# Kernel optimization log

Measured on AMD Instinct MI355X. Metric: run time of the kernel, lower is better.

Reference implementation:

```python
import jax, jax.numpy as jnp
import numpy as np

N_SPIKES = 1_000_000
N_UNITS = 400
N_NEIGHB = 64
C = 3        # n_candidates
S = 2        # n_search per candidate
E = 1        # n_explore


def setup_inputs() -> dict:
    key = jax.random.key(0)
    k1, k2, k3, k4 = jax.random.split(key, 4)
    top_candidates = jax.random.randint(k1, (N_SPIKES, C), 0, N_UNITS, dtype=jnp.int32)
    unit_search_neighbors = jax.random.randint(k2, (N_UNITS, S), 0, N_UNITS, dtype=jnp.int32)
    neighborhood_ids = jax.random.randint(k3, (N_SPIKES,), 0, N_NEIGHB, dtype=jnp.int32)
    unit_logliks = jax.random.normal(k4, (N_UNITS,), dtype=jnp.float32)
    return {
        "unit_logliks": unit_logliks,
        "top_candidates": top_candidates,
        "unit_search_neighbors": unit_search_neighbors,
        "neighborhood_ids": neighborhood_ids,
    }


def _propose(top, usn, nb):
    """Deterministic JAX version of CandidateSet.propose_candidates.

    top: (n, C) int top candidate units per spike (invariant 1)
    usn: (U, S) int search neighbors per unit
    nb:  (n,)   int neighborhood id per spike
    Returns: candidates (n, C + C*S + E) with dups erased to -1,
             unit_neighborhood_counts (U, N_NEIGHB).
    """
    n = top.shape[0]
    U = usn.shape[0]
    # search candidates: gather neighbors of each top candidate -> (n, C*S)
    search = usn[top].reshape(n, C * S)
    # scatter-add counts of best unit per neighborhood (np.add.at equivalent)
    counts = jnp.zeros((U, N_NEIGHB), jnp.int32).at[top[:, 0], nb].add(1)
    # units_overlapping_neighborhoods: per neighborhood, sorted unit ids with
    # count > 0, padded with sentinel U -> (N_NEIGHB, U)
    overlap = counts.T > 0                                  # (N_NEIGHB, U)
    explore_units = jnp.sort(jnp.where(overlap, jnp.arange(U, dtype=jnp.int32), U), axis=1)
    # searchsorted(row, U) == number of valid entries per neighborhood
    n_explore = overlap.sum(axis=1).astype(jnp.int32)       # (N_NEIGHB,)
    ne = n_explore[nb]                                      # (n,)
    # integers_without_inner_replacement with E=1: uniform index in [0, ne)
    u = jax.random.uniform(jax.random.key(1), (n, E))
    targs = jnp.floor(u * ne[:, None].astype(u.dtype)).astype(jnp.int32)
    targs = jnp.where(ne[:, None] > 0, jnp.minimum(targs, ne[:, None] - 1), -1)
    explore = explore_units[nb[:, None], jnp.maximum(targs, 0)]
    explore = jnp.where(targs < 0, -1, explore)             # (n, E)
    candidates = jnp.concatenate([top, search, explore], axis=1)  # (n, T)
    # second scatter-add: all non-top columns (negatives masked out)
    tail = candidates[:, 1:]
    valid = tail >= 0
    counts = counts.at[jnp.where(valid, tail, 0), jnp.where(valid, nb[:, None], 0)].add(
        valid.astype(jnp.int32)
    )
    # erase_dups: keep first occurrence in each row, later dups -> -1
    T = candidates.shape[1]
    eq = candidates[:, :, None] == candidates[:, None, :]   # (n, T, T)
    earlier = jnp.tril(jnp.ones((T, T), bool), k=-1)        # [j, i] with i < j
    dup = (eq & earlier).any(axis=2)
    candidates = jnp.where(dup, -1, candidates)
    return candidates, counts


def reference(unit_logliks, top_candidates, unit_search_neighbors, neighborhood_ids):
    candidates, counts = _propose(top_candidates, unit_search_neighbors, neighborhood_ids)
    # per-candidate loglik gather (the float gather used by the E step)
    scores = jnp.where(candidates >= 0, unit_logliks[jnp.maximum(candidates, 0)], 0.0)
    return candidates, counts, scores
```

## Files before the change

### kernel.cpp

```cpp
#include <hip/hip_runtime.h>
#include <stdint.h>

#define N_UNITS   400
#define N_NEIGHB  64
#define C         3
#define S         2
#define T         10
#define NSLICE_A  128
#define HALF_NB   32
#define HH        (HALF_NB * N_UNITS)
#define EH        (N_UNITS * 32)
#define BS        256
#define MB        512

__device__ __forceinline__ uint32_t rotl32(uint32_t x, int d) {
    return (x << d) | (x >> (32 - d));
}

__device__ __forceinline__ void threefry_key01(uint32_t x0, uint32_t x1,
                                               uint32_t& o0, uint32_t& o1) {
    const uint32_t ks0 = 0u;
    const uint32_t ks1 = 1u;
    const uint32_t ks2 = 0x1BD11BDBu;
    x0 += ks0; x1 += ks1;
#define TF_RND(r) { x0 += x1; x1 = rotl32(x1, r); x1 ^= x0; }
    TF_RND(13) TF_RND(15) TF_RND(26) TF_RND(6)
    x0 += ks1; x1 += ks2 + 1u;
    TF_RND(17) TF_RND(29) TF_RND(16) TF_RND(24)
    x0 += ks2; x1 += ks0 + 2u;
    TF_RND(13) TF_RND(15) TF_RND(26) TF_RND(6)
    x0 += ks0; x1 += ks1 + 3u;
    TF_RND(17) TF_RND(29) TF_RND(16) TF_RND(24)
    x0 += ks1; x1 += ks2 + 4u;
    TF_RND(13) TF_RND(15) TF_RND(26) TF_RND(6)
    x0 += ks2; x1 += ks0 + 5u;
#undef TF_RND
    o0 = x0; o1 = x1;
}

__device__ __forceinline__ int explore_index(int i, int ne) {
    uint32_t o0, o1;
    threefry_key01(0u, (uint32_t)i, o0, o1);
    uint32_t bits = o0 ^ o1;
    float u = __uint_as_float((bits >> 9) | 0x3F800000u) - 1.0f;
    int t = (int)floorf(u * (float)ne);
    return min(t, ne - 1);
}

__global__ void k_histA(const int* __restrict__ top,
                        const int* __restrict__ nbid,
                        uint32_t* __restrict__ PA, int n, int chunk) {
    __shared__ uint32_t hist[HH];
    for (int k = threadIdx.x; k < HH; k += blockDim.x) hist[k] = 0u;
    __syncthreads();
    int h = blockIdx.x & 1, s = blockIdx.x >> 1;
    int lo = s * chunk, hi = min(n, lo + chunk);
    const int4* top4 = (const int4*)top;
#define PROC(nb, t0, t1, t2) if (((nb) >> 5) == h) { \
    int r = ((nb) & 31) * N_UNITS; \
    atomicAdd(&hist[r + (t0)], 1u); \
    atomicAdd(&hist[r + (t1)], 0x10000u); \
    atomicAdd(&hist[r + (t2)], 0x10000u); }
    for (int i0 = lo + threadIdx.x * 4; i0 < hi; i0 += blockDim.x * 4) {
        if (i0 + 4 <= hi) {
            int4 nb4 = *(const int4*)(nbid + i0);
            int j = (i0 * 3) >> 2;
            int4 ta = top4[j], tb = top4[j + 1], tc = top4[j + 2];
            PROC(nb4.x, ta.x, ta.y, ta.z)
            PROC(nb4.y, ta.w, tb.x, tb.y)
            PROC(nb4.z, tb.z, tb.w, tc.x)
            PROC(nb4.w, tc.y, tc.z, tc.w)
        } else {
            for (int i = i0; i < hi; ++i)
                PROC(nbid[i], top[3 * i], top[3 * i + 1], top[3 * i + 2])
        }
    }
#undef PROC
    __syncthreads();
    uint32_t* Pb = PA + (size_t)blockIdx.x * HH;
    for (int k = threadIdx.x; k < HH; k += blockDim.x) Pb[k] = hist[k];
}

__global__ void k_tables_base(const uint32_t* __restrict__ PA,
                              const int* __restrict__ usn,
                              int* __restrict__ wtbl,
                              int* __restrict__ wne,
                              float* __restrict__ out_counts) {
    __shared__ int scan[512];
    __shared__ int s_c[N_UNITS];
    __shared__ int s_h3[N_UNITS];
    int b = blockIdx.x, u = threadIdx.x;
    int h = b >> 5;
    int base = (b & 31) * N_UNITS;
    int h0 = 0, h12 = 0;
    if (u < N_UNITS) {
#pragma unroll 8
        for (int s = 0; s < NSLICE_A; ++s) {
            uint32_t w = PA[(size_t)(s * 2 + h) * HH + base + u];
            h0  += (int)(w & 0xFFFFu);
            h12 += (int)(w >> 16);
        }
        int h3 = h0 + h12;
        s_h3[u] = h3;
        s_c[u] = h3;
    }
    int p = (u < N_UNITS && h0 > 0) ? 1 : 0;
    scan[u] = p;
    __syncthreads();
    for (int off = 1; off < 512; off <<= 1) {
        int add = (u >= off) ? scan[u - off] : 0;
        __syncthreads();
        scan[u] += add;
        __syncthreads();
    }
    if (p) wtbl[b * N_UNITS + scan[u] - 1] = u;
    if (u == 511) wne[b] = scan[511];
    if (u < N_UNITS) {
        int h3 = s_h3[u];
        if (h3 > 0) {
            int2 nbr = ((const int2*)usn)[u];
            atomicAdd(&s_c[nbr.x], h3);
            atomicAdd(&s_c[nbr.y], h3);
        }
    }
    __syncthreads();
    if (u < N_UNITS)
        out_counts[u * N_NEIGHB + b] = (float)s_c[u];
}

__global__ void k_main(const float* __restrict__ logliks,
                       const int* __restrict__ top,
                       const int* __restrict__ usn,
                       const int* __restrict__ nbid,
                       const int* __restrict__ wtbl,
                       const int* __restrict__ wne,
                       uint32_t* __restrict__ PD,
                       float* __restrict__ out_cand,
                       float* __restrict__ out_scores,
                       int n, int chunk) {
    __shared__ uint32_t hist[EH];
    __shared__ int   s_usn[N_UNITS * S];
    __shared__ float s_ll[N_UNITS];
    __shared__ int   s_ne[N_NEIGHB];
    int tid = threadIdx.x;
    for (int k = tid; k < EH; k += BS) hist[k] = 0u;
    for (int k = tid; k < N_UNITS * S; k += BS) s_usn[k] = usn[k];
    for (int k = tid; k < N_UNITS; k += BS)     s_ll[k]  = logliks[k];
    for (int k = tid; k < N_NEIGHB; k += BS)    s_ne[k]  = wne[k];
    __syncthreads();

    int lo = blockIdx.x * chunk, hi = min(n, lo + chunk);
    for (int i = lo + tid; i < hi; i += BS) {
        int nb = nbid[i];
        int cand[T];
        cand[0] = top[i * 3 + 0];
        cand[1] = top[i * 3 + 1];
        cand[2] = top[i * 3 + 2];
#pragma unroll
        for (int c = 0; c < C; ++c) {
            cand[C + 2 * c]     = s_usn[cand[c] * 2 + 0];
            cand[C + 2 * c + 1] = s_usn[cand[c] * 2 + 1];
        }
        int ne = s_ne[nb];
        if (ne > 0) {
            int t = explore_index(i, ne);
            int ex = wtbl[nb * N_UNITS + t];
            cand[T - 1] = ex;
            atomicAdd(&hist[ex * 32 + (nb >> 1)], (nb & 1) ? 0x10000u : 1u);
        } else {
            cand[T - 1] = -1;
        }

        float vc[T], vs[T];
#pragma unroll
        for (int jj = 0; jj < T; ++jj) {
            bool dup = false;
#pragma unroll
            for (int k = 0; k < jj; ++k) dup |= (cand[k] == cand[jj]);
            int v = dup ? -1 : cand[jj];
            vc[jj] = (float)v;
            vs[jj] = (v >= 0) ? s_ll[v] : 0.0f;
        }
        float2* oc2 = (float2*)(out_cand   + (size_t)i * T);
        float2* os2 = (float2*)(out_scores + (size_t)i * T);
#pragma unroll
        for (int jj = 0; jj < T / 2; ++jj) {
            oc2[jj] = make_float2(vc[2 * jj], vc[2 * jj + 1]);
            os2[jj] = make_float2(vs[2 * jj], vs[2 * jj + 1]);
        }
    }
    __syncthreads();
    uint32_t* Pb = PD + (size_t)blockIdx.x * EH;
    for (int k = tid; k < EH; k += BS) Pb[k] = hist[k];
}

__global__ void k_finalE(const uint32_t* __restrict__ PD,
                         float* __restrict__ out_counts) {
    __shared__ uint32_t red[256];
    int tid = threadIdx.x;
    int wl = tid & 63, g = tid >> 6;
    int w = blockIdx.x * 64 + wl;
    uint32_t sum = 0;
#pragma unroll 8
    for (int s = g * (MB / 4); s < (g + 1) * (MB / 4); ++s)
        sum += PD[(size_t)s * EH + w];
    red[tid] = sum;
    __syncthreads();
    if (g == 0) {
        uint32_t tot = red[wl] + red[wl + 64] + red[wl + 128] + red[wl + 192];
        int u = w >> 5, nb2 = (w & 31) * 2;
        float2* p = (float2*)(out_counts + u * N_NEIGHB + nb2);
        float2 v = *p;
        v.x += (float)(tot & 0xFFFFu);
        v.y += (float)(tot >> 16);
        *p = v;
    }
}

extern "C" void kernel_launch(void* const* d_in, const int* in_sizes, int n_in,
                              void* d_out, int out_size, void* d_ws, size_t ws_size,
                              hipStream_t stream) {
    const float* logliks = (const float*)d_in[0];
    const int*   top     = (const int*)d_in[1];
    const int*   usn     = (const int*)d_in[2];
    const int*   nbid    = (const int*)d_in[3];

    int n = in_sizes[3];
    int chunkA = ((n + NSLICE_A - 1) / NSLICE_A + 3) & ~3;
    int chunkM = (n + MB - 1) / MB;

    float* out        = (float*)d_out;
    float* out_cand   = out;
    float* out_counts = out + (size_t)n * T;
    float* out_scores = out_counts + (size_t)N_UNITS * N_NEIGHB;

    int*      wtbl = (int*)d_ws;
    int*      wne  = wtbl + N_NEIGHB * N_UNITS;
    uint32_t* PA   = (uint32_t*)(wne + 64);
    uint32_t* PD   = PA + (size_t)NSLICE_A * 2 * HH;

    k_histA      <<<NSLICE_A * 2, BS, 0, stream>>>(top, nbid, PA, n, chunkA);
    k_tables_base<<<N_NEIGHB, 512, 0, stream>>>(PA, usn, wtbl, wne, out_counts);
    k_main       <<<MB, BS, 0, stream>>>(logliks, top, usn, nbid, wtbl, wne,
                                         PD, out_cand, out_scores, n, chunkM);
    k_finalE     <<<EH / 64, BS, 0, stream>>>(PD, out_counts);
}
```

Baseline: 144.9 us.

## Stage top-candidate loads and output rows through shared memory for coalescing

The main kernel now processes spikes in tiles of 256. It loads each tile's top candidates with coalesced int4 reads into shared memory, writes the per-spike candidate and score rows into shared buffers, then stores them with contiguous float4 writes. Per-block chunks are rounded up to a multiple of the block size. The aim is to replace strided per-thread 12-byte loads and 40-byte-stride float2 stores with fully coalesced transfers. The cost is two extra barriers per tile and about 23KB more shared memory per block, which may lower occupancy.

```diff
diff --git a/kernel.cpp b/kernel.cpp
--- a/kernel.cpp
+++ b/kernel.cpp
@@ -142,6 +142,9 @@
     __shared__ int   s_usn[N_UNITS * S];
     __shared__ float s_ll[N_UNITS];
     __shared__ int   s_ne[N_NEIGHB];
+    __shared__ int   s_top[BS * 3];
+    __shared__ float s_bc[BS * T];
+    __shared__ float s_bs[BS * T];
     int tid = threadIdx.x;
     for (int k = tid; k < EH; k += BS) hist[k] = 0u;
     for (int k = tid; k < N_UNITS * S; k += BS) s_usn[k] = usn[k];
@@ -150,43 +153,61 @@
     __syncthreads();
 
     int lo = blockIdx.x * chunk, hi = min(n, lo + chunk);
-    for (int i = lo + tid; i < hi; i += BS) {
-        int nb = nbid[i];
-        int cand[T];
-        cand[0] = top[i * 3 + 0];
-        cand[1] = top[i * 3 + 1];
-        cand[2] = top[i * 3 + 2];
+    for (int t0 = lo; t0 < hi; t0 += BS) {
+        int cnt = min(BS, hi - t0);
+        if (cnt == BS) {
+            if (tid < (BS * 3) / 4)
+                ((int4*)s_top)[tid] = ((const int4*)(top + (size_t)t0 * 3))[tid];
+        } else {
+            for (int k = tid; k < cnt * 3; k += BS)
+                s_top[k] = top[(size_t)t0 * 3 + k];
+        }
+        __syncthreads();
+
+        int i = t0 + tid;
+        if (i < hi) {
+            int nb = nbid[i];
+            int cand[T];
+            cand[0] = s_top[tid * 3 + 0];
+            cand[1] = s_top[tid * 3 + 1];
+            cand[2] = s_top[tid * 3 + 2];
 #pragma unroll
-        for (int c = 0; c < C; ++c) {
-            cand[C + 2 * c]     = s_usn[cand[c] * 2 + 0];
-            cand[C + 2 * c + 1] = s_usn[cand[c] * 2 + 1];
-        }
-        int ne = s_ne[nb];
-        if (ne > 0) {
-            int t = explore_index(i, ne);
-            int ex = wtbl[nb * N_UNITS + t];
-            cand[T - 1] = ex;
-            atomicAdd(&hist[ex * 32 + (nb >> 1)], (nb & 1) ? 0x10000u : 1u);
-        } else {
-            cand[T - 1] = -1;
-        }
-
-        float vc[T], vs[T];
+            for (int c = 0; c < C; ++c) {
+                cand[C + 2 * c]     = s_usn[cand[c] * 2 + 0];
+                cand[C + 2 * c + 1] = s_usn[cand[c] * 2 + 1];
+            }
+            int ne = s_ne[nb];
+            if (ne > 0) {
+                int t = explore_index(i, ne);
+                int ex = wtbl[nb * N_UNITS + t];
+                cand[T - 1] = ex;
+                atomicAdd(&hist[ex * 32 + (nb >> 1)], (nb & 1) ? 0x10000u : 1u);
+            } else {
+                cand[T - 1] = -1;
+            }
 #pragma unroll
-        for (int jj = 0; jj < T; ++jj) {
-            bool dup = false;
+            for (int jj = 0; jj < T; ++jj) {
+                bool dup = false;
 #pragma unroll
-            for (int k = 0; k < jj; ++k) dup |= (cand[k] == cand[jj]);
-            int v = dup ? -1 : cand[jj];
-            vc[jj] = (float)v;
-            vs[jj] = (v >= 0) ? s_ll[v] : 0.0f;
-        }
-        float2* oc2 = (float2*)(out_cand   + (size_t)i * T);
-        float2* os2 = (float2*)(out_scores + (size_t)i * T);
-#pragma unroll
-        for (int jj = 0; jj < T / 2; ++jj) {
-            oc2[jj] = make_float2(vc[2 * jj], vc[2 * jj + 1]);
-            os2[jj] = make_float2(vs[2 * jj], vs[2 * jj + 1]);
+                for (int k = 0; k < jj; ++k) dup |= (cand[k] == cand[jj]);
+                int v = dup ? -1 : cand[jj];
+                s_bc[tid * T + jj] = (float)v;
+                s_bs[tid * T + jj] = (v >= 0) ? s_ll[v] : 0.0f;
+            }
+        }
+        __syncthreads();
+
+        int nfloat = cnt * T;
+        float* oc = out_cand   + (size_t)t0 * T;
+        float* os = out_scores + (size_t)t0 * T;
+        int nvec = nfloat & ~3;
+        for (int e = tid * 4; e < nvec; e += BS * 4) {
+            *(float4*)(oc + e) = *(const float4*)(s_bc + e);
+            *(float4*)(os + e) = *(const float4*)(s_bs + e);
+        }
+        for (int e = nvec + tid; e < nfloat; e += BS) {
+            oc[e] = s_bc[e];
+            os[e] = s_bs[e];
         }
     }
     __syncthreads();
@@ -227,7 +248,7 @@
 
     int n = in_sizes[3];
     int chunkA = ((n + NSLICE_A - 1) / NSLICE_A + 3) & ~3;
-    int chunkM = (n + MB - 1) / MB;
+    int chunkM = (((n + MB - 1) / MB) + BS - 1) & ~(BS - 1);
 
     float* out        = (float*)d_out;
     float* out_cand   = out;
```

New measurement: 143.8 us. About the same (-0.7%).

## Fuse four kernels into one cooperative kernel with grid-wide syncs

Applied to the files above, without the earlier changes.

Replaces the four separate launches (histogram, table build, main candidate pass, final count reduction) with a single cooperative kernel that separates the phases with grid.sync(). It also doubles the number of histogram slices and adds a separate grid-wide partial-sum phase before the per-neighborhood table build. The aim is to remove launch gaps and per-kernel startup overhead. In exchange it adds grid barriers and more global partial-histogram traffic, and it depends on all 512 blocks being co-resident, falling back to the old launches if the cooperative launch fails.

```diff
diff --git a/kernel.cpp b/kernel.cpp
--- a/kernel.cpp
+++ b/kernel.cpp
@@ -1,16 +1,23 @@
 #include <hip/hip_runtime.h>
+#include <hip/hip_cooperative_groups.h>
 #include <stdint.h>
+
+namespace cg = cooperative_groups;
 
 #define N_UNITS   400
 #define N_NEIGHB  64
 #define C         3
 #define S         2
 #define T         10
-#define NSLICE_A  128
+#define BS        256
+#define GB        512
+#define SLICE_A   256
 #define HALF_NB   32
 #define HH        (HALF_NB * N_UNITS)
 #define EH        (N_UNITS * 32)
-#define BS        256
+#define SMEMW     14064
+
+#define NSLICE_A  128
 #define MB        512
 
 __device__ __forceinline__ uint32_t rotl32(uint32_t x, int d) {
@@ -45,6 +52,192 @@
     float u = __uint_as_float((bits >> 9) | 0x3F800000u) - 1.0f;
     int t = (int)floorf(u * (float)ne);
     return min(t, ne - 1);
+}
+
+__global__ __launch_bounds__(BS, 2)
+void k_fused(const float* __restrict__ logliks,
+             const int* __restrict__ top,
+             const int* __restrict__ usn,
+             const int* __restrict__ nbid,
+             int* __restrict__ wtbl, int* __restrict__ wne,
+             uint32_t* __restrict__ PA, uint32_t* __restrict__ PD,
+             uint32_t* __restrict__ Hsum,
+             float* out_counts,
+             float* __restrict__ out_cand,
+             float* __restrict__ out_scores,
+             int n, int chunkA, int chunkM) {
+    __shared__ uint32_t smem[SMEMW];
+    cg::grid_group grid = cg::this_grid();
+    int tid = threadIdx.x;
+    int b = blockIdx.x;
+
+    {
+        uint32_t* hist = smem;
+        for (int k = tid; k < HH; k += BS) hist[k] = 0u;
+        __syncthreads();
+        int h = b & 1, s = b >> 1;
+        int lo = s * chunkA, hi = min(n, lo + chunkA);
+        const int4* top4 = (const int4*)top;
+#define PROC(nb, t0, t1, t2) if (((nb) >> 5) == h) { \
+    int r = ((nb) & 31) * N_UNITS; \
+    atomicAdd(&hist[r + (t0)], 1u); \
+    atomicAdd(&hist[r + (t1)], 0x10000u); \
+    atomicAdd(&hist[r + (t2)], 0x10000u); }
+        for (int i0 = lo + tid * 4; i0 < hi; i0 += BS * 4) {
+            if (i0 + 4 <= hi) {
+                int4 nb4 = *(const int4*)(nbid + i0);
+                int j = (i0 * 3) >> 2;
+                int4 ta = top4[j], tb = top4[j + 1], tc = top4[j + 2];
+                PROC(nb4.x, ta.x, ta.y, ta.z)
+                PROC(nb4.y, ta.w, tb.x, tb.y)
+                PROC(nb4.z, tb.z, tb.w, tc.x)
+                PROC(nb4.w, tc.y, tc.z, tc.w)
+            } else {
+                for (int i = i0; i < hi; ++i)
+                    PROC(nbid[i], top[3 * i], top[3 * i + 1], top[3 * i + 2])
+            }
+        }
+#undef PROC
+        __syncthreads();
+        uint32_t* Pb = PA + (size_t)b * HH;
+        for (int k = tid; k < HH; k += BS) Pb[k] = hist[k];
+    }
+    __threadfence();
+    grid.sync();
+
+    {
+        int c = b * BS + tid;
+        if (c < N_NEIGHB * N_UNITS) {
+            int nb = c / N_UNITS, u = c - nb * N_UNITS;
+            int h = nb >> 5, base = (nb & 31) * N_UNITS + u;
+            uint32_t sum = 0;
+#pragma unroll 8
+            for (int s = 0; s < SLICE_A; ++s)
+                sum += PA[(size_t)(s * 2 + h) * HH + base];
+            Hsum[c] = sum;
+        }
+    }
+    __threadfence();
+    grid.sync();
+
+    if (b < N_NEIGHB) {
+        uint32_t* bufA = smem;
+        uint32_t* bufB = smem + 512;
+        int* s_c  = (int*)(smem + 1024);
+        int* s_h3 = (int*)(smem + 1536);
+        int* s_p  = (int*)(smem + 2048);
+        for (int u = tid; u < N_UNITS; u += BS) {
+            uint32_t w = Hsum[b * N_UNITS + u];
+            int h0 = (int)(w & 0xFFFFu), h12 = (int)(w >> 16);
+            int h3 = h0 + h12;
+            s_h3[u] = h3;
+            s_c[u]  = h3;
+            s_p[u]  = (h0 > 0) ? 1 : 0;
+            bufA[u] = (uint32_t)s_p[u];
+        }
+        __syncthreads();
+        uint32_t* src = bufA; uint32_t* dst = bufB;
+        for (int off = 1; off < 512; off <<= 1) {
+            for (int u = tid; u < N_UNITS; u += BS)
+                dst[u] = src[u] + ((u >= off) ? src[u - off] : 0u);
+            __syncthreads();
+            uint32_t* t = src; src = dst; dst = t;
+        }
+        for (int u = tid; u < N_UNITS; u += BS)
+            if (s_p[u]) wtbl[b * N_UNITS + (int)src[u] - 1] = u;
+        if (tid == 0) wne[b] = (int)src[N_UNITS - 1];
+        __syncthreads();
+        for (int u = tid; u < N_UNITS; u += BS) {
+            int h3 = s_h3[u];
+            if (h3 > 0) {
+                int2 nbr = ((const int2*)usn)[u];
+                atomicAdd(&s_c[nbr.x], h3);
+                atomicAdd(&s_c[nbr.y], h3);
+            }
+        }
+        __syncthreads();
+        for (int u = tid; u < N_UNITS; u += BS)
+            out_counts[u * N_NEIGHB + b] = (float)s_c[u];
+    }
+    __threadfence();
+    grid.sync();
+
+    {
+        uint32_t* hist  = smem;
+        int*      s_usn = (int*)(smem + EH);
+        float*    s_ll  = (float*)(smem + EH + 800);
+        int*      s_ne  = (int*)(smem + EH + 1200);
+        for (int k = tid; k < EH; k += BS) hist[k] = 0u;
+        for (int k = tid; k < N_UNITS * S; k += BS) s_usn[k] = usn[k];
+        for (int k = tid; k < N_UNITS; k += BS)     s_ll[k]  = logliks[k];
+        for (int k = tid; k < N_NEIGHB; k += BS)    s_ne[k]  = wne[k];
+        __syncthreads();
+        int lo = b * chunkM, hi = min(n, lo + chunkM);
+        for (int i = lo + tid; i < hi; i += BS) {
+            int nb = nbid[i];
+            int cand[T];
+            cand[0] = top[i * 3 + 0];
+            cand[1] = top[i * 3 + 1];
+            cand[2] = top[i * 3 + 2];
+#pragma unroll
+            for (int c = 0; c < C; ++c) {
+                cand[C + 2 * c]     = s_usn[cand[c] * 2 + 0];
+                cand[C + 2 * c + 1] = s_usn[cand[c] * 2 + 1];
+            }
+            int ne = s_ne[nb];
+            if (ne > 0) {
+                int t = explore_index(i, ne);
+                int ex = wtbl[nb * N_UNITS + t];
+                cand[T - 1] = ex;
+                atomicAdd(&hist[ex * 32 + (nb >> 1)], (nb & 1) ? 0x10000u : 1u);
+            } else {
+                cand[T - 1] = -1;
+            }
+            float vc[T], vs[T];
+#pragma unroll
+            for (int jj = 0; jj < T; ++jj) {
+                bool dup = false;
+#pragma unroll
+                for (int k = 0; k < jj; ++k) dup |= (cand[k] == cand[jj]);
+                int v = dup ? -1 : cand[jj];
+                vc[jj] = (float)v;
+                vs[jj] = (v >= 0) ? s_ll[v] : 0.0f;
+            }
+            float2* oc2 = (float2*)(out_cand   + (size_t)i * T);
+            float2* os2 = (float2*)(out_scores + (size_t)i * T);
+#pragma unroll
+            for (int jj = 0; jj < T / 2; ++jj) {
+                oc2[jj] = make_float2(vc[2 * jj], vc[2 * jj + 1]);
+                os2[jj] = make_float2(vs[2 * jj], vs[2 * jj + 1]);
+            }
+        }
+        __syncthreads();
+        uint32_t* Pb = PD + (size_t)b * EH;
+        for (int k = tid; k < EH; k += BS) Pb[k] = hist[k];
+    }
+    __threadfence();
+    grid.sync();
+
+    if (b < EH / 64) {
+        uint32_t* red = smem;
+        int wl = tid & 63, g = tid >> 6;
+        int w = b * 64 + wl;
+        uint32_t sum = 0;
+#pragma unroll 8
+        for (int s = g * (GB / 4); s < (g + 1) * (GB / 4); ++s)
+            sum += PD[(size_t)s * EH + w];
+        red[tid] = sum;
+        __syncthreads();
+        if (g == 0) {
+            uint32_t tot = red[wl] + red[wl + 64] + red[wl + 128] + red[wl + 192];
+            int u = w >> 5, nb2 = (w & 31) * 2;
+            float2* p = (float2*)(out_counts + u * N_NEIGHB + nb2);
+            float2 v = *p;
+            v.x += (float)(tot & 0xFFFFu);
+            v.y += (float)(tot >> 16);
+            *p = v;
+        }
+    }
 }
 
 __global__ void k_histA(const int* __restrict__ top,
@@ -148,7 +341,6 @@
     for (int k = tid; k < N_UNITS; k += BS)     s_ll[k]  = logliks[k];
     for (int k = tid; k < N_NEIGHB; k += BS)    s_ne[k]  = wne[k];
     __syncthreads();
-
     int lo = blockIdx.x * chunk, hi = min(n, lo + chunk);
     for (int i = lo + tid; i < hi; i += BS) {
         int nb = nbid[i];
@@ -170,7 +362,6 @@
         } else {
             cand[T - 1] = -1;
         }
-
         float vc[T], vs[T];
 #pragma unroll
         for (int jj = 0; jj < T; ++jj) {
@@ -226,8 +417,6 @@
     const int*   nbid    = (const int*)d_in[3];
 
     int n = in_sizes[3];
-    int chunkA = ((n + NSLICE_A - 1) / NSLICE_A + 3) & ~3;
-    int chunkM = (n + MB - 1) / MB;
 
     float* out        = (float*)d_out;
     float* out_cand   = out;
@@ -237,8 +426,25 @@
     int*      wtbl = (int*)d_ws;
     int*      wne  = wtbl + N_NEIGHB * N_UNITS;
     uint32_t* PA   = (uint32_t*)(wne + 64);
-    uint32_t* PD   = PA + (size_t)NSLICE_A * 2 * HH;
-
+    uint32_t* PD   = PA + (size_t)GB * HH;
+    uint32_t* Hsum = PD + (size_t)GB * EH;
+
+    int chunkA_f = ((n + SLICE_A - 1) / SLICE_A + 3) & ~3;
+    int chunkM_f = (n + GB - 1) / GB;
+
+    void* args[] = { (void*)&logliks, (void*)&top, (void*)&usn, (void*)&nbid,
+                     (void*)&wtbl, (void*)&wne, (void*)&PA, (void*)&PD,
+                     (void*)&Hsum, (void*)&out_counts, (void*)&out_cand,
+                     (void*)&out_scores, (void*)&n, (void*)&chunkA_f,
+                     (void*)&chunkM_f };
+    hipError_t rc = hipLaunchCooperativeKernel((const void*)k_fused,
+                                               dim3(GB), dim3(BS),
+                                               args, 0, stream);
+    if (rc == hipSuccess) return;
+    (void)hipGetLastError();
+
+    int chunkA = ((n + NSLICE_A - 1) / NSLICE_A + 3) & ~3;
+    int chunkM = (n + MB - 1) / MB;
     k_histA      <<<NSLICE_A * 2, BS, 0, stream>>>(top, nbid, PA, n, chunkA);
     k_tables_base<<<N_NEIGHB, 512, 0, stream>>>(PA, usn, wtbl, wne, out_counts);
     k_main       <<<MB, BS, 0, stream>>>(logliks, top, usn, nbid, wtbl, wne,
```

New measurement: 579.1 us. +299.7%, slower.
